# Optimization experiments

Hardware: AMD Instinct MI355X
Metric: run time of the kernel (lower is better)

## Reference

```python
import jax, jax.numpy as jnp
import numpy as np

LN_EPS = 1e-5

def setup_inputs() -> dict:
    key = jax.random.key(0)
    ks = jax.random.split(key, 6)
    N, CD, CC, CF = 500000, 64, 96, 128
    return {
        "x_detial": jax.random.normal(ks[0], (N, CD), dtype=jnp.float32),
        "x_context": jax.random.normal(ks[1], (N, CC), dtype=jnp.float32),
        "W_detial": jax.random.normal(ks[2], (CD, CF), dtype=jnp.float32) * 0.05,
        "W_context": jax.random.normal(ks[3], (CC, CF), dtype=jnp.float32) * 0.05,
        "W_gate1": jax.random.normal(ks[4], (CD + CC, CF // 2), dtype=jnp.float32) * 0.05,
        "ln_gamma": jnp.ones((CF // 2,), dtype=jnp.float32),
        "ln_beta": jnp.zeros((CF // 2,), dtype=jnp.float32),
        "W_gate2": jax.random.normal(ks[5], (CF // 2, 1), dtype=jnp.float32) * 0.05,
    }

def _layer_norm(x, gamma, beta):
    mu = jnp.mean(x, axis=-1, keepdims=True)
    var = jnp.mean(jnp.square(x - mu), axis=-1, keepdims=True)
    return (x - mu) * jax.lax.rsqrt(var + LN_EPS) * gamma + beta

def reference(x_detial, x_context, W_detial, W_context, W_gate1, ln_gamma, ln_beta, W_gate2):
    # gate path: 1x1 subm conv == per-point linear on [N, C] features
    concat = jnp.concatenate([x_detial, x_context], axis=1)        # [N, CD+CC]
    h = jnp.matmul(concat, W_gate1)                                 # [N, CF//2]
    h = jax.nn.relu(_layer_norm(h, ln_gamma, ln_beta))
    gate = jax.nn.sigmoid(jnp.matmul(h, W_gate2))                   # [N, 1]
    detail_aligned = jnp.matmul(x_detial, W_detial)                 # [N, CF]
    context_aligned = jnp.matmul(x_context, W_context)              # [N, CF]
    return (1.0 - gate) * context_aligned + gate * detail_aligned   # [N, CF]
```

## Files before the change

### kernel.cpp

```cpp
#include <hip/hip_runtime.h>
#include <hip/hip_bf16.h>
#include <math.h>


namespace {

typedef __attribute__((ext_vector_type(8))) short short8;
typedef __attribute__((ext_vector_type(4))) float f32x4;

constexpr int CD = 64, CC = 96, CH = 64, CF = 128;
constexpr int NFG1 = 20;
constexpr int NFCB = 40;
constexpr int NFRAG = NFG1 + NFCB;
constexpr int WCH_ALL = NFRAG * 512 * 2 / 16;

__device__ inline short bf16_of(float f) {
  __hip_bfloat16 h = __float2bfloat16(f);
  return *reinterpret_cast<short*>(&h);
}

__global__ void convert_weights(const float* __restrict__ Wd,
                                const float* __restrict__ Wc,
                                const float* __restrict__ Wg1,
                                short* __restrict__ ws) {
  const int t = blockIdx.x * 256 + threadIdx.x;
  if (t >= 64 * NFRAG) return;
  const int frag = t >> 6, l = t & 63;
  const int cidx = l & 15, kb = l >> 4;
  float v[8];
  if (frag < NFG1) {
    const int ks = frag >> 2, nt = frag & 3;
    const int n = nt * 16 + cidx;
    #pragma unroll
    for (int j = 0; j < 8; ++j) {
      const int k = ks * 32 + (j >> 2) * 16 + kb * 4 + (j & 3);
      v[j] = Wg1[k * CH + n];
    }
  } else {
    const int f2 = frag - NFG1;
    const int ks = f2 >> 3, nt = f2 & 7;
    const int n = nt * 16 + cidx;
    #pragma unroll
    for (int j = 0; j < 8; ++j) {
      const int k = ks * 32 + (j >> 2) * 16 + kb * 4 + (j & 3);
      v[j] = (k < CD) ? Wd[k * CF + n] : Wc[(k - CD) * CF + n];
    }
  }
  short8 o;
  #pragma unroll
  for (int j = 0; j < 8; ++j) o[j] = bf16_of(v[j]);
  *reinterpret_cast<short8*>(ws + frag * 512 + l * 8) = o;
}

#define BURST(p0,p1,p2,p3,p4,p5,p6,p7,p8,p9, rdp, rcp)                 \
  asm volatile(                                                        \
      "global_load_dwordx4 %0, %[ad], off\n\t"                         \
      "global_load_dwordx4 %1, %[ad], off offset:64\n\t"               \
      "global_load_dwordx4 %2, %[ad], off offset:128\n\t"              \
      "global_load_dwordx4 %3, %[ad], off offset:192\n\t"              \
      "global_load_dwordx4 %4, %[ac], off\n\t"                         \
      "global_load_dwordx4 %5, %[ac], off offset:64\n\t"               \
      "global_load_dwordx4 %6, %[ac], off offset:128\n\t"              \
      "global_load_dwordx4 %7, %[ac], off offset:192\n\t"              \
      "global_load_dwordx4 %8, %[ac], off offset:256\n\t"              \
      "global_load_dwordx4 %9, %[ac], off offset:320"                  \
      : "=&v"(p0), "=&v"(p1), "=&v"(p2), "=&v"(p3), "=&v"(p4),         \
        "=&v"(p5), "=&v"(p6), "=&v"(p7), "=&v"(p8), "=&v"(p9)          \
      : [ad] "v"(rdp), [ac] "v"(rcp)                                   \
      : "memory")

#define WAITB(N, p0,p1,p2,p3,p4,p5,p6,p7,p8,p9)                        \
  asm volatile("s_waitcnt vmcnt(" #N ")"                               \
      : "+v"(p0), "+v"(p1), "+v"(p2), "+v"(p3), "+v"(p4),              \
        "+v"(p5), "+v"(p6), "+v"(p7), "+v"(p8), "+v"(p9)               \
      :: "memory")

__global__ __launch_bounds__(512)
void gate_fusion_mfma(const float* __restrict__ xd,
                      const float* __restrict__ xc,
                      const float* __restrict__ gma,
                      const float* __restrict__ bta,
                      const float* __restrict__ Wg2,
                      const short* __restrict__ wf,
                      float* __restrict__ out, int nTiles) {
  __shared__ short wlds[NFRAG * 512];

  const int tid  = threadIdx.x;
  const int lane = tid & 63;
  const int wv   = tid >> 6;
  const int cidx = lane & 15;
  const int kb   = lane >> 4;
  const int tb   = (blockIdx.x * 8 + wv) * 4;

  for (int c = tid; c < WCH_ALL; c += 512) {
    short8 v = *reinterpret_cast<const short8*>(wf + (size_t)c * 8);
    *reinterpret_cast<short8*>(&wlds[c * 8]) = v;
  }
  __syncthreads();

  float gmv[4], btv[4], w2v[4];
  #pragma unroll
  for (int nt = 0; nt < 4; ++nt) {
    const int c = nt * 16 + cidx;
    gmv[nt] = gma[c]; btv[nt] = bta[c]; w2v[nt] = Wg2[c];
  }

  const f32x4 vzero = {0.f, 0.f, 0.f, 0.f};

  auto addrD = [&](int t) {
    const int tc = (t < nTiles) ? t : (nTiles - 1);
    return xd + ((size_t)tc * 16 + cidx) * CD + kb * 4;
  };
  auto addrC = [&](int t) {
    const int tc = (t < nTiles) ? t : (nTiles - 1);
    return xc + ((size_t)tc * 16 + cidx) * CC + kb * 4;
  };

  auto compute = [&](int t, const f32x4& l0, const f32x4& h0,
                     const f32x4& l1, const f32x4& h1,
                     const f32x4& l2, const f32x4& h2,
                     const f32x4& l3, const f32x4& h3,
                     const f32x4& l4, const f32x4& h4) {
    const int r0 = t * 16;
    const f32x4 lo[5] = {l0, l1, l2, l3, l4};
    const f32x4 hi[5] = {h0, h1, h2, h3, h4};
    short8 xf[5];
    #pragma unroll
    for (int ks = 0; ks < 5; ++ks) {
      short8 f;
      #pragma unroll
      for (int j = 0; j < 4; ++j) {
        f[j]     = bf16_of(lo[ks][j]);
        f[4 + j] = bf16_of(hi[ks][j]);
      }
      xf[ks] = f;
    }

    f32x4 acc1[4];
    #pragma unroll
    for (int nt = 0; nt < 4; ++nt) acc1[nt] = vzero;
    #pragma unroll
    for (int ks = 0; ks < 5; ++ks) {
      short8 bg[4];
      #pragma unroll
      for (int nt = 0; nt < 4; ++nt)
        bg[nt] = *reinterpret_cast<const short8*>(
            &wlds[(ks * 4 + nt) * 512 + lane * 8]);
      #pragma unroll
      for (int nt = 0; nt < 4; ++nt)
        acc1[nt] = __builtin_amdgcn_mfma_f32_16x16x32_bf16(
            xf[ks], bg[nt], acc1[nt], 0, 0, 0);
    }

    float gate[4];
    {
      float s[4], q[4];
      #pragma unroll
      for (int r = 0; r < 4; ++r) {
        s[r] = 0.f; q[r] = 0.f;
        #pragma unroll
        for (int nt = 0; nt < 4; ++nt) {
          const float c = acc1[nt][r];
          s[r] += c; q[r] += c * c;
        }
      }
      #pragma unroll
      for (int m = 1; m < 16; m <<= 1)
        #pragma unroll
        for (int r = 0; r < 4; ++r) {
          s[r] += __shfl_xor(s[r], m, 64);
          q[r] += __shfl_xor(q[r], m, 64);
        }
      float p[4];
      #pragma unroll
      for (int r = 0; r < 4; ++r) {
        const float mu  = s[r] * (1.f / CH);
        const float var = q[r] * (1.f / CH) - mu * mu;
        const float rsd = rsqrtf(var + 1e-5f);
        float pp = 0.f;
        #pragma unroll
        for (int nt = 0; nt < 4; ++nt) {
          const float h = fmaxf((acc1[nt][r] - mu) * rsd * gmv[nt] + btv[nt], 0.f);
          pp += h * w2v[nt];
        }
        p[r] = pp;
      }
      #pragma unroll
      for (int m = 1; m < 16; m <<= 1)
        #pragma unroll
        for (int r = 0; r < 4; ++r) p[r] += __shfl_xor(p[r], m, 64);
      #pragma unroll
      for (int r = 0; r < 4; ++r) gate[r] = 1.f / (1.f + expf(-p[r]));
    }

    #pragma unroll
    for (int q = 0; q < 4; ++q) {
      f32x4 aD[2], aC[2];
      #pragma unroll
      for (int nt = 0; nt < 2; ++nt) { aD[nt] = vzero; aC[nt] = vzero; }
      #pragma unroll
      for (int ks = 0; ks < 5; ++ks) {
        short8 bg[2];
        #pragma unroll
        for (int nt = 0; nt < 2; ++nt)
          bg[nt] = *reinterpret_cast<const short8*>(
              &wlds[(NFG1 + ks * 8 + q * 2 + nt) * 512 + lane * 8]);
        if (ks < 2) {
          #pragma unroll
          for (int nt = 0; nt < 2; ++nt)
            aD[nt] = __builtin_amdgcn_mfma_f32_16x16x32_bf16(
                xf[ks], bg[nt], aD[nt], 0, 0, 0);
        } else {
          #pragma unroll
          for (int nt = 0; nt < 2; ++nt)
            aC[nt] = __builtin_amdgcn_mfma_f32_16x16x32_bf16(
                xf[ks], bg[nt], aC[nt], 0, 0, 0);
        }
      }
      const size_t rowb = (size_t)r0 + kb * 4;
      #pragma unroll
      for (int nt = 0; nt < 2; ++nt) {
        #pragma unroll
        for (int r = 0; r < 4; ++r) {
          const float g = gate[r];
          const float o = fmaf(g, aD[nt][r] - aC[nt][r], aC[nt][r]);
          out[(rowb + r) * CF + (q * 2 + nt) * 16 + cidx] = o;
        }
      }
    }
  };

  f32x4 a0, a1, a2, a3, a4, a5, a6, a7, a8, a9;
  f32x4 b0, b1, b2, b3, b4, b5, b6, b7, b8, b9;

  BURST(a0,a1,a2,a3,a4,a5,a6,a7,a8,a9, addrD(tb),     addrC(tb));
  BURST(b0,b1,b2,b3,b4,b5,b6,b7,b8,b9, addrD(tb + 1), addrC(tb + 1));

  WAITB(10, a0,a1,a2,a3,a4,a5,a6,a7,a8,a9);
  if (tb < nTiles)     compute(tb,     a0,a1, a2,a3, a4,a5, a6,a7, a8,a9);

  BURST(a0,a1,a2,a3,a4,a5,a6,a7,a8,a9, addrD(tb + 2), addrC(tb + 2));
  WAITB(10, b0,b1,b2,b3,b4,b5,b6,b7,b8,b9);
  if (tb + 1 < nTiles) compute(tb + 1, b0,b1, b2,b3, b4,b5, b6,b7, b8,b9);

  BURST(b0,b1,b2,b3,b4,b5,b6,b7,b8,b9, addrD(tb + 3), addrC(tb + 3));
  WAITB(10, a0,a1,a2,a3,a4,a5,a6,a7,a8,a9);
  if (tb + 2 < nTiles) compute(tb + 2, a0,a1, a2,a3, a4,a5, a6,a7, a8,a9);

  WAITB(0, b0,b1,b2,b3,b4,b5,b6,b7,b8,b9);
  if (tb + 3 < nTiles) compute(tb + 3, b0,b1, b2,b3, b4,b5, b6,b7, b8,b9);
}

}

extern "C" void kernel_launch(void* const* d_in, const int* in_sizes, int n_in,
                              void* d_out, int out_size, void* d_ws, size_t ws_size,
                              hipStream_t stream) {
  const float* xd  = (const float*)d_in[0];
  const float* xc  = (const float*)d_in[1];
  const float* Wd  = (const float*)d_in[2];
  const float* Wc  = (const float*)d_in[3];
  const float* Wg1 = (const float*)d_in[4];
  const float* gma = (const float*)d_in[5];
  const float* bta = (const float*)d_in[6];
  const float* Wg2 = (const float*)d_in[7];
  float* out = (float*)d_out;
  short* ws  = (short*)d_ws;

  const int N = in_sizes[0] / CD;
  const int nTiles = N / 16;

  convert_weights<<<dim3(15), dim3(256), 0, stream>>>(Wd, Wc, Wg1, ws);

  const int tilesPerBlock = 8 * 4;
  const int nblk = (nTiles + tilesPerBlock - 1) / tilesPerBlock;
  gate_fusion_mfma<<<dim3(nblk), dim3(512), 0, stream>>>(
      xd, xc, gma, bta, Wg2, ws, out, nTiles);
}
```

Before: 131.5 us.

## Transpose MFMA output for vectorized nontemporal stores and halve per-wave rows

Swaps the MFMA operand order so each lane holds four contiguous output columns of one row. Every lane then writes a single 16-byte nontemporal store, replacing the earlier scattered scalar stores. To support this, the gate value is redistributed across lanes with shuffles. Each wave now processes 32 rows (two tiles) instead of 64, doubling the grid size. The LayerNorm/gate parameter loads are folded into the first inline-asm load burst and broadcast with shuffles, and the tail guard is simplified to an early return for inactive waves. Risks are less latency hiding per wave, extra shuffle work, and reliance on vmcnt ordering across mixed loads and stores.

After: 134.9 us. +2.5%, slower.

```diff
diff --git a/kernel.cpp b/kernel.cpp
--- a/kernel.cpp
+++ b/kernel.cpp
@@ -52,7 +52,29 @@
   *reinterpret_cast<short8*>(ws + frag * 512 + l * 8) = o;
 }
 
-#define BURST(p0,p1,p2,p3,p4,p5,p6,p7,p8,p9, rdp, rcp)                 \
+#define BURSTA(p0,p1,p2,p3,p4,p5,p6,p7,p8,p9, g0,g1,g2, rdp, rcp, pg, pb, pw) \
+  asm volatile(                                                        \
+      "global_load_dwordx4 %0, %[ad], off\n\t"                         \
+      "global_load_dwordx4 %1, %[ad], off offset:64\n\t"               \
+      "global_load_dwordx4 %2, %[ad], off offset:128\n\t"              \
+      "global_load_dwordx4 %3, %[ad], off offset:192\n\t"              \
+      "global_load_dwordx4 %4, %[ac], off\n\t"                         \
+      "global_load_dwordx4 %5, %[ac], off offset:64\n\t"               \
+      "global_load_dwordx4 %6, %[ac], off offset:128\n\t"              \
+      "global_load_dwordx4 %7, %[ac], off offset:192\n\t"              \
+      "global_load_dwordx4 %8, %[ac], off offset:256\n\t"              \
+      "global_load_dwordx4 %9, %[ac], off offset:320\n\t"              \
+      "global_load_dword %[og], %[sg], off\n\t"                        \
+      "global_load_dword %[ob], %[sb], off\n\t"                        \
+      "global_load_dword %[ow], %[sw], off"                            \
+      : "=&v"(p0), "=&v"(p1), "=&v"(p2), "=&v"(p3), "=&v"(p4),         \
+        "=&v"(p5), "=&v"(p6), "=&v"(p7), "=&v"(p8), "=&v"(p9),         \
+        [og] "=&v"(g0), [ob] "=&v"(g1), [ow] "=&v"(g2)                 \
+      : [ad] "v"(rdp), [ac] "v"(rcp), [sg] "v"(pg), [sb] "v"(pb),      \
+        [sw] "v"(pw)                                                   \
+      : "memory")
+
+#define BURSTB(p0,p1,p2,p3,p4,p5,p6,p7,p8,p9, rdp, rcp)                \
   asm volatile(                                                        \
       "global_load_dwordx4 %0, %[ad], off\n\t"                         \
       "global_load_dwordx4 %1, %[ad], off offset:64\n\t"               \
@@ -69,7 +91,14 @@
       : [ad] "v"(rdp), [ac] "v"(rcp)                                   \
       : "memory")
 
-#define WAITB(N, p0,p1,p2,p3,p4,p5,p6,p7,p8,p9)                        \
+#define WAITA(N, p0,p1,p2,p3,p4,p5,p6,p7,p8,p9, g0,g1,g2)              \
+  asm volatile("s_waitcnt vmcnt(" #N ")"                               \
+      : "+v"(p0), "+v"(p1), "+v"(p2), "+v"(p3), "+v"(p4),              \
+        "+v"(p5), "+v"(p6), "+v"(p7), "+v"(p8), "+v"(p9),              \
+        "+v"(g0), "+v"(g1), "+v"(g2)                                   \
+      :: "memory")
+
+#define WAITN(N, p0,p1,p2,p3,p4,p5,p6,p7,p8,p9)                        \
   asm volatile("s_waitcnt vmcnt(" #N ")"                               \
       : "+v"(p0), "+v"(p1), "+v"(p2), "+v"(p3), "+v"(p4),              \
         "+v"(p5), "+v"(p6), "+v"(p7), "+v"(p8), "+v"(p9)               \
@@ -82,7 +111,7 @@
                       const float* __restrict__ bta,
                       const float* __restrict__ Wg2,
                       const short* __restrict__ wf,
-                      float* __restrict__ out, int nTiles) {
+                      float* __restrict__ out, int N) {
   __shared__ short wlds[NFRAG * 512];
 
   const int tid  = threadIdx.x;
@@ -90,40 +119,20 @@
   const int wv   = tid >> 6;
   const int cidx = lane & 15;
   const int kb   = lane >> 4;
-  const int tb   = (blockIdx.x * 8 + wv) * 4;
+  const int r0   = blockIdx.x * 256 + wv * 32;
+  const bool active = (r0 < N);
 
   for (int c = tid; c < WCH_ALL; c += 512) {
     short8 v = *reinterpret_cast<const short8*>(wf + (size_t)c * 8);
     *reinterpret_cast<short8*>(&wlds[c * 8]) = v;
   }
   __syncthreads();
-
-  float gmv[4], btv[4], w2v[4];
-  #pragma unroll
-  for (int nt = 0; nt < 4; ++nt) {
-    const int c = nt * 16 + cidx;
-    gmv[nt] = gma[c]; btv[nt] = bta[c]; w2v[nt] = Wg2[c];
-  }
+  if (!active) return;
 
   const f32x4 vzero = {0.f, 0.f, 0.f, 0.f};
 
-  auto addrD = [&](int t) {
-    const int tc = (t < nTiles) ? t : (nTiles - 1);
-    return xd + ((size_t)tc * 16 + cidx) * CD + kb * 4;
-  };
-  auto addrC = [&](int t) {
-    const int tc = (t < nTiles) ? t : (nTiles - 1);
-    return xc + ((size_t)tc * 16 + cidx) * CC + kb * 4;
-  };
-
-  auto compute = [&](int t, const f32x4& l0, const f32x4& h0,
-                     const f32x4& l1, const f32x4& h1,
-                     const f32x4& l2, const f32x4& h2,
-                     const f32x4& l3, const f32x4& h3,
-                     const f32x4& l4, const f32x4& h4) {
-    const int r0 = t * 16;
-    const f32x4 lo[5] = {l0, l1, l2, l3, l4};
-    const f32x4 hi[5] = {h0, h1, h2, h3, h4};
+  auto compute = [&](int rr0, const f32x4* lo, const f32x4* hi,
+                     const float* gmv, const float* btv, const float* w2v) {
     short8 xf[5];
     #pragma unroll
     for (int ks = 0; ks < 5; ++ks) {
@@ -193,62 +202,70 @@
       for (int r = 0; r < 4; ++r) gate[r] = 1.f / (1.f + expf(-p[r]));
     }
 
-    #pragma unroll
-    for (int q = 0; q < 4; ++q) {
-      f32x4 aD[2], aC[2];
-      #pragma unroll
-      for (int nt = 0; nt < 2; ++nt) { aD[nt] = vzero; aC[nt] = vzero; }
+    float g4[4];
+    #pragma unroll
+    for (int r = 0; r < 4; ++r) g4[r] = __shfl(gate[r], (cidx >> 2) << 4);
+    const int rs = cidx & 3;
+    const float g_row = rs == 3 ? g4[3] : rs == 2 ? g4[2] : rs == 1 ? g4[1] : g4[0];
+
+    #pragma unroll
+    for (int s = 0; s < 8; ++s) {
+      f32x4 aD = vzero, aC = vzero;
       #pragma unroll
       for (int ks = 0; ks < 5; ++ks) {
-        short8 bg[2];
-        #pragma unroll
-        for (int nt = 0; nt < 2; ++nt)
-          bg[nt] = *reinterpret_cast<const short8*>(
-              &wlds[(NFG1 + ks * 8 + q * 2 + nt) * 512 + lane * 8]);
-        if (ks < 2) {
-          #pragma unroll
-          for (int nt = 0; nt < 2; ++nt)
-            aD[nt] = __builtin_amdgcn_mfma_f32_16x16x32_bf16(
-                xf[ks], bg[nt], aD[nt], 0, 0, 0);
-        } else {
-          #pragma unroll
-          for (int nt = 0; nt < 2; ++nt)
-            aC[nt] = __builtin_amdgcn_mfma_f32_16x16x32_bf16(
-                xf[ks], bg[nt], aC[nt], 0, 0, 0);
-        }
-      }
-      const size_t rowb = (size_t)r0 + kb * 4;
-      #pragma unroll
-      for (int nt = 0; nt < 2; ++nt) {
-        #pragma unroll
-        for (int r = 0; r < 4; ++r) {
-          const float g = gate[r];
-          const float o = fmaf(g, aD[nt][r] - aC[nt][r], aC[nt][r]);
-          out[(rowb + r) * CF + (q * 2 + nt) * 16 + cidx] = o;
-        }
-      }
+        short8 bg = *reinterpret_cast<const short8*>(
+            &wlds[(NFG1 + ks * 8 + s) * 512 + lane * 8]);
+        if (ks < 2)
+          aD = __builtin_amdgcn_mfma_f32_16x16x32_bf16(bg, xf[ks], aD, 0, 0, 0);
+        else
+          aC = __builtin_amdgcn_mfma_f32_16x16x32_bf16(bg, xf[ks], aC, 0, 0, 0);
+      }
+      f32x4 o;
+      #pragma unroll
+      for (int r = 0; r < 4; ++r) o[r] = fmaf(g_row, aD[r] - aC[r], aC[r]);
+      float* dst = &out[((size_t)rr0 + cidx) * CF + s * 16 + kb * 4];
+      asm volatile("global_store_dwordx4 %0, %1, off nt"
+                   :: "v"(dst), "v"(o) : "memory");
     }
   };
 
-  f32x4 a0, a1, a2, a3, a4, a5, a6, a7, a8, a9;
-  f32x4 b0, b1, b2, b3, b4, b5, b6, b7, b8, b9;
-
-  BURST(a0,a1,a2,a3,a4,a5,a6,a7,a8,a9, addrD(tb),     addrC(tb));
-  BURST(b0,b1,b2,b3,b4,b5,b6,b7,b8,b9, addrD(tb + 1), addrC(tb + 1));
-
-  WAITB(10, a0,a1,a2,a3,a4,a5,a6,a7,a8,a9);
-  if (tb < nTiles)     compute(tb,     a0,a1, a2,a3, a4,a5, a6,a7, a8,a9);
-
-  BURST(a0,a1,a2,a3,a4,a5,a6,a7,a8,a9, addrD(tb + 2), addrC(tb + 2));
-  WAITB(10, b0,b1,b2,b3,b4,b5,b6,b7,b8,b9);
-  if (tb + 1 < nTiles) compute(tb + 1, b0,b1, b2,b3, b4,b5, b6,b7, b8,b9);
-
-  BURST(b0,b1,b2,b3,b4,b5,b6,b7,b8,b9, addrD(tb + 3), addrC(tb + 3));
-  WAITB(10, a0,a1,a2,a3,a4,a5,a6,a7,a8,a9);
-  if (tb + 2 < nTiles) compute(tb + 2, a0,a1, a2,a3, a4,a5, a6,a7, a8,a9);
-
-  WAITB(0, b0,b1,b2,b3,b4,b5,b6,b7,b8,b9);
-  if (tb + 3 < nTiles) compute(tb + 3, b0,b1, b2,b3, b4,b5, b6,b7, b8,b9);
+  f32x4 a0,a1,a2,a3,a4,a5,a6,a7,a8,a9, b0,b1,b2,b3,b4,b5,b6,b7,b8,b9;
+  float gaL, baL, waL;
+  {
+    const float* rdp0 = xd + ((size_t)r0 + cidx) * CD + kb * 4;
+    const float* rcp0 = xc + ((size_t)r0 + cidx) * CC + kb * 4;
+    BURSTA(a0,a1,a2,a3,a4,a5,a6,a7,a8,a9, gaL,baL,waL,
+           rdp0, rcp0, gma + lane, bta + lane, Wg2 + lane);
+    const float* rdp1 = xd + ((size_t)r0 + 16 + cidx) * CD + kb * 4;
+    const float* rcp1 = xc + ((size_t)r0 + 16 + cidx) * CC + kb * 4;
+    BURSTB(b0,b1,b2,b3,b4,b5,b6,b7,b8,b9, rdp1, rcp1);
+  }
+
+  WAITA(10, a0,a1,a2,a3,a4,a5,a6,a7,a8,a9, gaL,baL,waL);
+  __builtin_amdgcn_sched_barrier(0);
+
+  float gmv[4], btv[4], w2v[4];
+  #pragma unroll
+  for (int nt = 0; nt < 4; ++nt) {
+    gmv[nt] = __shfl(gaL, nt * 16 + cidx);
+    btv[nt] = __shfl(baL, nt * 16 + cidx);
+    w2v[nt] = __shfl(waL, nt * 16 + cidx);
+  }
+
+  {
+    const f32x4 lo0[5] = {a0, a2, a4, a6, a8};
+    const f32x4 hi0[5] = {a1, a3, a5, a7, a9};
+    compute(r0, lo0, hi0, gmv, btv, w2v);
+  }
+
+  WAITN(8, b0,b1,b2,b3,b4,b5,b6,b7,b8,b9);
+  __builtin_amdgcn_sched_barrier(0);
+
+  {
+    const f32x4 lo1[5] = {b0, b2, b4, b6, b8};
+    const f32x4 hi1[5] = {b1, b3, b5, b7, b9};
+    compute(r0 + 16, lo1, hi1, gmv, btv, w2v);
+  }
 }
 
 }
@@ -268,12 +285,10 @@
   short* ws  = (short*)d_ws;
 
   const int N = in_sizes[0] / CD;
-  const int nTiles = N / 16;
 
   convert_weights<<<dim3(15), dim3(256), 0, stream>>>(Wd, Wc, Wg1, ws);
 
-  const int tilesPerBlock = 8 * 4;
-  const int nblk = (nTiles + tilesPerBlock - 1) / tilesPerBlock;
+  const int nblk = (N + 255) / 256;
   gate_fusion_mfma<<<dim3(nblk), dim3(512), 0, stream>>>(
-      xd, xc, gma, bta, Wg2, ws, out, nTiles);
-}
+      xd, xc, gma, bta, Wg2, ws, out, N);
+}
```
